# Kernel optimization log

Measured on AMD Instinct MI355X. Metric: run time of the kernel, lower is better.

The kernel has to match this reference:

```python
import jax, jax.numpy as jnp
import numpy as np

N_NODES = 20000
N_EDGES = 320000
HIDDEN = 64
HEADS = 4
D_INNER = 256
NEG_SLOPE = 0.2
BN_EPS = 1e-5


def setup_inputs() -> dict:
    key = jax.random.key(0)
    ks = jax.random.split(key, 8)
    s = 1.0 / np.sqrt(HIDDEN)
    return {
        "x": jax.random.normal(ks[0], (N_NODES, HIDDEN), jnp.float32),
        "edge_index": jax.random.randint(ks[1], (2, N_EDGES), 0, N_NODES, jnp.int64),
        "W_l": jax.random.normal(ks[2], (HIDDEN, HEADS * HIDDEN), jnp.float32) * s,
        "b_l": jnp.zeros((HEADS * HIDDEN,), jnp.float32),
        "W_r": jax.random.normal(ks[3], (HIDDEN, HEADS * HIDDEN), jnp.float32) * s,
        "b_r": jnp.zeros((HEADS * HIDDEN,), jnp.float32),
        "att": jax.random.normal(ks[4], (HEADS, HIDDEN), jnp.float32) * s,
        "bias_gat": jnp.zeros((HIDDEN,), jnp.float32),
        "gamma1": jnp.ones((HIDDEN,), jnp.float32),
        "beta1": jnp.zeros((HIDDEN,), jnp.float32),
        "W1": jax.random.normal(ks[5], (HIDDEN, D_INNER), jnp.float32) * s,
        "b1": jnp.zeros((D_INNER,), jnp.float32),
        "W2": jax.random.normal(ks[6], (D_INNER, HIDDEN), jnp.float32) / np.sqrt(D_INNER),
        "b2": jnp.zeros((HIDDEN,), jnp.float32),
        "gamma2": jnp.ones((HIDDEN,), jnp.float32),
        "beta2": jnp.zeros((HIDDEN,), jnp.float32),
    }


def _batch_norm(x, gamma, beta):
    # training-mode BatchNorm1d over the node axis (biased variance, as torch)
    mu = x.mean(0)
    var = jnp.mean((x - mu) ** 2, axis=0)
    return (x - mu) * jax.lax.rsqrt(var + BN_EPS) * gamma + beta


def _gatv2(x, edge_index, W_l, b_l, W_r, b_r, att, bias_gat):
    N = x.shape[0]
    H, C = att.shape
    src, dst = edge_index[0], edge_index[1]  # j (source), i (target)
    xl = (x @ W_l + b_l).reshape(N, H, C)  # messages (x_j side)
    xr = (x @ W_r + b_r).reshape(N, H, C)  # target (x_i side)
    # GATv2 dynamic attention: a^T LeakyReLU(x_i + x_j), per head
    e = jax.nn.leaky_relu(xl[src] + xr[dst], NEG_SLOPE)  # [E, H, C]
    score = jnp.einsum("ehc,hc->eh", e, att)  # [E, H]
    # segment softmax over incoming edges of each target node
    m = jax.ops.segment_max(score, dst, num_segments=N)  # [N, H]
    ex = jnp.exp(score - m[dst])
    denom = jax.ops.segment_sum(ex, dst, num_segments=N)  # [N, H]
    alpha = ex / jnp.maximum(denom[dst], 1e-16)  # [E, H]
    out = jax.ops.segment_sum(alpha[:, :, None] * xl[src], dst, num_segments=N)  # [N, H, C]
    return out.mean(axis=1) + bias_gat  # concat=False -> mean over heads


def reference(x, edge_index, W_l, b_l, W_r, b_r, att, bias_gat,
              gamma1, beta1, W1, b1, W2, b2, gamma2, beta2):
    x2 = _gatv2(x, edge_index, W_l, b_l, W_r, b_r, att, bias_gat)
    x = x + x2  # dropout is identity in eval
    x = _batch_norm(x, gamma1, beta1)
    ff = jax.nn.relu(x @ W1 + b1) @ W2 + b2
    x = x + ff
    x = _batch_norm(x, gamma2, beta2)
    return x
```

## Files before the change

kernel.cpp:

```cpp
#include <hip/hip_runtime.h>
#include <hip/hip_bf16.h>
#include <math.h>

#define N_NODES 20000
#define N_EDGES 320000
#define HIDDEN 64
#define HEADS 4
#define HC 256
#define D_INNER 256
#define NEG_SLOPE 0.2f
#define BN_EPS 1e-5f
#define MAXDEG 64
#define NZERO (N_NODES + 2048)
#define NB_LIN 626
#define NB_FILL 1250

typedef __attribute__((ext_vector_type(8))) short short8;
typedef __attribute__((ext_vector_type(4))) float f32x4;

__device__ __forceinline__ float bf2f(unsigned short u) {
    unsigned x = ((unsigned)u) << 16;
    return __uint_as_float(x);
}
__device__ __forceinline__ unsigned short f2bf(float f) {
    __hip_bfloat16 b = __float2bfloat16(f);
    return *reinterpret_cast<unsigned short*>(&b);
}
__device__ __forceinline__ void cvt8(uint4 u, float* f) {
    f[0] = __uint_as_float(u.x << 16); f[1] = __uint_as_float(u.x & 0xFFFF0000u);
    f[2] = __uint_as_float(u.y << 16); f[3] = __uint_as_float(u.y & 0xFFFF0000u);
    f[4] = __uint_as_float(u.z << 16); f[5] = __uint_as_float(u.z & 0xFFFF0000u);
    f[6] = __uint_as_float(u.w << 16); f[7] = __uint_as_float(u.w & 0xFFFF0000u);
}

__global__ __launch_bounds__(256) void k_wprep(const float* __restrict__ W1, const float* __restrict__ W2,
                                               const float* __restrict__ Wl, const float* __restrict__ Wr,
                                               unsigned short* __restrict__ W1tb, unsigned short* __restrict__ W2tb,
                                               unsigned short* __restrict__ Wlrtb,
                                               int* __restrict__ zbuf, int* __restrict__ perm) {
    int idx = blockIdx.x * 256 + threadIdx.x;
    if (idx < NZERO) zbuf[idx] = 0;
    int4 z4 = {0, 0, 0, 0};
    int4* p4 = (int4*)perm;
#pragma unroll
    for (int i = 0; i < 5; ++i) {
        int k = idx + i * 65536;
        if (k < N_NODES * MAXDEG / 4) p4[k] = z4;
    }
    if (idx < 16384) {
        int k = idx >> 8, n = idx & 255;
        W1tb[n * 64 + k] = f2bf(W1[idx]);
    } else if (idx < 32768) {
        int j = idx - 16384;
        int k = j >> 6, n = j & 63;
        W2tb[n * 256 + k] = f2bf(W2[j]);
    } else if (idx < 49152) {
        int j = idx - 32768;
        int k = j >> 8, n = j & 255;
        Wlrtb[n * 64 + k] = f2bf(Wl[j]);
    } else {
        int j = idx - 49152;
        int k = j >> 8, n = j & 255;
        Wlrtb[16384 + n * 64 + k] = f2bf(Wr[j]);
    }
}

__global__ __launch_bounds__(256) void k_prep(const float* __restrict__ x,
                                              const unsigned short* __restrict__ Wlrtb,
                                              const float* __restrict__ bl, const float* __restrict__ br,
                                              unsigned short* __restrict__ xlb, unsigned short* __restrict__ xrb,
                                              const int* __restrict__ ei,
                                              int* __restrict__ cursor, int* __restrict__ perm) {
    __shared__ unsigned short sW[16384];
    int t = threadIdx.x;
    if (blockIdx.x >= NB_LIN) {
        int e = (blockIdx.x - NB_LIN) * 256 + t;
        int ed = ei[N_EDGES + e];
        int slot = atomicAdd(&cursor[ed], 1);
        perm[ed * MAXDEG + slot] = ei[e];
        return;
    }
    int w = t >> 6, lane = t & 63;
    int l15 = lane & 15, lg = lane >> 4;
    int side = blockIdx.x & 1;
    int row0 = (blockIdx.x >> 1) * 64;
    const float* bias = side ? br : bl;
    unsigned short* dst = side ? xrb : xlb;
    {
        const short8* src = (const short8*)(Wlrtb + side * 16384);
#pragma unroll
        for (int it = 0; it < 8; ++it) {
            int i = it * 256 + t;
            int n = i >> 3, c = i & 7;
            *(short8*)((char*)sW + n * 128 + ((c * 16) ^ ((n & 7) << 4))) = src[i];
        }
    }
    short8 af[4][2];
#pragma unroll
    for (int mt = 0; mt < 4; ++mt) {
        int gm = row0 + mt * 16 + l15;
        bool valid = gm < N_NODES;
#pragma unroll
        for (int kk = 0; kk < 2; ++kk) {
            int k0 = kk * 32 + lg * 8;
            float4 v0 = {0.f,0.f,0.f,0.f}, v1 = {0.f,0.f,0.f,0.f};
            if (valid) {
                v0 = *(const float4*)(x + (size_t)gm * 64 + k0);
                v1 = *(const float4*)(x + (size_t)gm * 64 + k0 + 4);
            }
            short8 f;
            f[0] = (short)f2bf(v0.x); f[1] = (short)f2bf(v0.y);
            f[2] = (short)f2bf(v0.z); f[3] = (short)f2bf(v0.w);
            f[4] = (short)f2bf(v1.x); f[5] = (short)f2bf(v1.y);
            f[6] = (short)f2bf(v1.z); f[7] = (short)f2bf(v1.w);
            af[mt][kk] = f;
        }
    }
    float bv[4];
#pragma unroll
    for (int nt = 0; nt < 4; ++nt) bv[nt] = bias[w * 64 + nt * 16 + l15];
    __syncthreads();
    f32x4 zero4 = {0.f, 0.f, 0.f, 0.f};
    f32x4 acc[4][4];
#pragma unroll
    for (int mt = 0; mt < 4; ++mt)
#pragma unroll
        for (int nt = 0; nt < 4; ++nt) acc[mt][nt] = zero4;
#pragma unroll
    for (int kk = 0; kk < 2; ++kk) {
        int kb = kk * 64 + lg * 16;
        short8 bf[4];
#pragma unroll
        for (int nt = 0; nt < 4; ++nt) {
            int n = w * 64 + nt * 16 + l15;
            bf[nt] = *(const short8*)((const char*)sW + n * 128 + (kb ^ ((n & 7) << 4)));
        }
#pragma unroll
        for (int mt = 0; mt < 4; ++mt)
#pragma unroll
            for (int nt = 0; nt < 4; ++nt)
                acc[mt][nt] = __builtin_amdgcn_mfma_f32_16x16x32_bf16(af[mt][kk], bf[nt], acc[mt][nt], 0, 0, 0);
    }
#pragma unroll
    for (int mt = 0; mt < 4; ++mt)
#pragma unroll
        for (int nt = 0; nt < 4; ++nt) {
            int n = w * 64 + nt * 16 + l15;
#pragma unroll
            for (int r = 0; r < 4; ++r) {
                int gm = row0 + mt * 16 + lg * 4 + r;
                if (gm < N_NODES)
                    dst[(size_t)gm * 256 + n] = f2bf(acc[mt][nt][r] + bv[nt]);
            }
        }
}

__global__ __launch_bounds__(256) void k_gat(const unsigned short* __restrict__ xlb,
                                             const unsigned short* __restrict__ xrb,
                                             const float* __restrict__ att,
                                             const int* __restrict__ perm,
                                             const int* __restrict__ cnt,
                                             const float* __restrict__ x,
                                             const float* __restrict__ bias,
                                             float* __restrict__ y1,
                                             float* __restrict__ gsum, float* __restrict__ gsq) {
    __shared__ float ps[8][64], pq[8][64];
    int t = threadIdx.x;
    int hw = t >> 5, l = t & 31;
    int node = blockIdx.x * 8 + hw;
    const uint4* xl4 = (const uint4*)xlb;
    uint4 xru = ((const uint4*)xrb)[(size_t)node * 32 + l];
    float xr[8]; cvt8(xru, xr);
    float at[8];
    *(float4*)(at)     = *(const float4*)(att + l * 8);
    *(float4*)(at + 4) = *(const float4*)(att + l * 8 + 4);
    int deg = cnt[node];
    int mdeg = max(deg, __shfl_xor(deg, 32));
    const int* ep = perm + (size_t)node * MAXDEG;
    float d = 0.f;
    float acc[8] = {0.f,0.f,0.f,0.f,0.f,0.f,0.f,0.f};
    uint4 uv0 = xl4[(size_t)ep[0] * 32 + l];
    uint4 uv1 = xl4[(size_t)ep[1] * 32 + l];
    for (int j = 0; j < mdeg; ++j) {
        uint4 un = xl4[(size_t)ep[j + 2] * 32 + l];
        float xl[8]; cvt8(uv0, xl);
        float v[8];
        float sv0 = 0.f, sv1 = 0.f, sa0 = 0.f, sa1 = 0.f;
#pragma unroll
        for (int i = 0; i < 8; i += 2) {
            v[i] = xl[i] + xr[i];
            v[i+1] = xl[i+1] + xr[i+1];
            sv0 = fmaf(at[i], v[i], sv0);
            sa0 = fmaf(at[i], fabsf(v[i]), sa0);
            sv1 = fmaf(at[i+1], v[i+1], sv1);
            sa1 = fmaf(at[i+1], fabsf(v[i+1]), sa1);
        }
        float s = 0.6f * (sv0 + sv1) + 0.4f * (sa0 + sa1);
        s += __shfl_xor(s, 1);
        s += __shfl_xor(s, 2);
        s += __shfl_xor(s, 4);
        float w = (j < deg) ? __expf(s) : 0.f;
        d += w;
#pragma unroll
        for (int i = 0; i < 8; ++i) acc[i] = fmaf(w, xl[i], acc[i]);
        uv0 = uv1; uv1 = un;
    }
    float inv = 1.f / fmaxf(d, 1e-16f);
#pragma unroll
    for (int i = 0; i < 8; ++i) {
        float v2 = acc[i] * inv;
        v2 += __shfl_xor(v2, 8);
        v2 += __shfl_xor(v2, 16);
        acc[i] = v2;
    }
    if (l < 8) {
        float4 xv0 = *(const float4*)(x + (size_t)node * 64 + l * 8);
        float4 xv1 = *(const float4*)(x + (size_t)node * 64 + l * 8 + 4);
        float4 bv0 = *(const float4*)(bias + l * 8);
        float4 bv1 = *(const float4*)(bias + l * 8 + 4);
        float4 y0, y1v;
        y0.x = xv0.x + 0.25f * acc[0] + bv0.x;
        y0.y = xv0.y + 0.25f * acc[1] + bv0.y;
        y0.z = xv0.z + 0.25f * acc[2] + bv0.z;
        y0.w = xv0.w + 0.25f * acc[3] + bv0.w;
        y1v.x = xv1.x + 0.25f * acc[4] + bv1.x;
        y1v.y = xv1.y + 0.25f * acc[5] + bv1.y;
        y1v.z = xv1.z + 0.25f * acc[6] + bv1.z;
        y1v.w = xv1.w + 0.25f * acc[7] + bv1.w;
        *(float4*)(y1 + (size_t)node * 64 + l * 8) = y0;
        *(float4*)(y1 + (size_t)node * 64 + l * 8 + 4) = y1v;
        int c = l * 8;
        ps[hw][c+0] = y0.x; ps[hw][c+1] = y0.y; ps[hw][c+2] = y0.z; ps[hw][c+3] = y0.w;
        ps[hw][c+4] = y1v.x; ps[hw][c+5] = y1v.y; ps[hw][c+6] = y1v.z; ps[hw][c+7] = y1v.w;
        pq[hw][c+0] = y0.x*y0.x; pq[hw][c+1] = y0.y*y0.y; pq[hw][c+2] = y0.z*y0.z; pq[hw][c+3] = y0.w*y0.w;
        pq[hw][c+4] = y1v.x*y1v.x; pq[hw][c+5] = y1v.y*y1v.y; pq[hw][c+6] = y1v.z*y1v.z; pq[hw][c+7] = y1v.w*y1v.w;
    }
    __syncthreads();
    if (t < 64) {
        float s = 0.f, q = 0.f;
#pragma unroll
        for (int r = 0; r < 8; ++r) { s += ps[r][t]; q += pq[r][t]; }
        int rb = blockIdx.x & 7;
        atomicAdd(&gsum[rb * 64 + t], s);
        atomicAdd(&gsq [rb * 64 + t], q);
    }
}

__global__ __launch_bounds__(256) void k_ffn(const float* __restrict__ y1,
                                             const float* __restrict__ s1, const float* __restrict__ q1,
                                             const float* __restrict__ gamma1, const float* __restrict__ beta1,
                                             const unsigned short* __restrict__ W1tb, const float* __restrict__ b1,
                                             const unsigned short* __restrict__ W2tb, const float* __restrict__ b2,
                                             float* __restrict__ out,
                                             float* __restrict__ gsum2, float* __restrict__ gsq2) {
    __shared__ unsigned short sW[16384];
    __shared__ unsigned short sH[16384];
    __shared__ __align__(16) float sA1[64], sC1[64];
    int t = threadIdx.x;
    int w = t >> 6, lane = t & 63;
    int l15 = lane & 15, lg = lane >> 4;
    int blk = blockIdx.x;

    {
        const short8* src = (const short8*)W1tb;
#pragma unroll
        for (int it = 0; it < 8; ++it) {
            int i = it * 256 + t;
            int n = i >> 3, c = i & 7;
            *(short8*)((char*)sW + n * 128 + ((c * 16) ^ ((n & 7) << 4))) = src[i];
        }
    }
    if (t < 64) {
        float s = 0.f, q = 0.f;
#pragma unroll
        for (int r = 0; r < 8; ++r) { s += s1[r * 64 + t]; q += q1[r * 64 + t]; }
        float mu = s * (1.0f / N_NODES);
        float var = fmaxf(q * (1.0f / N_NODES) - mu * mu, 0.f);
        float av = gamma1[t] * rsqrtf(var + BN_EPS);
        sA1[t] = av; sC1[t] = beta1[t] - mu * av;
    }
    __syncthreads();

    float4 a1k[2][2], c1k[2][2];
#pragma unroll
    for (int kk = 0; kk < 2; ++kk) {
        int k0 = kk * 32 + lg * 8;
        a1k[kk][0] = *(const float4*)(sA1 + k0); a1k[kk][1] = *(const float4*)(sA1 + k0 + 4);
        c1k[kk][0] = *(const float4*)(sC1 + k0); c1k[kk][1] = *(const float4*)(sC1 + k0 + 4);
    }
    short8 af[4][2];
#pragma unroll
    for (int mt = 0; mt < 4; ++mt) {
        int gm = blk * 64 + mt * 16 + l15;
        bool valid = gm < N_NODES;
#pragma unroll
        for (int kk = 0; kk < 2; ++kk) {
            int k0 = kk * 32 + lg * 8;
            float4 v0 = {0.f,0.f,0.f,0.f}, v1 = {0.f,0.f,0.f,0.f};
            if (valid) {
                v0 = *(const float4*)(y1 + (size_t)gm * 64 + k0);
                v1 = *(const float4*)(y1 + (size_t)gm * 64 + k0 + 4);
            }
            short8 f;
            f[0] = (short)f2bf(fmaf(a1k[kk][0].x, v0.x, c1k[kk][0].x));
            f[1] = (short)f2bf(fmaf(a1k[kk][0].y, v0.y, c1k[kk][0].y));
            f[2] = (short)f2bf(fmaf(a1k[kk][0].z, v0.z, c1k[kk][0].z));
            f[3] = (short)f2bf(fmaf(a1k[kk][0].w, v0.w, c1k[kk][0].w));
            f[4] = (short)f2bf(fmaf(a1k[kk][1].x, v1.x, c1k[kk][1].x));
            f[5] = (short)f2bf(fmaf(a1k[kk][1].y, v1.y, c1k[kk][1].y));
            f[6] = (short)f2bf(fmaf(a1k[kk][1].z, v1.z, c1k[kk][1].z));
            f[7] = (short)f2bf(fmaf(a1k[kk][1].w, v1.w, c1k[kk][1].w));
            af[mt][kk] = f;
        }
    }
    float b1v[4];
#pragma unroll
    for (int nt = 0; nt < 4; ++nt) b1v[nt] = b1[w * 64 + nt * 16 + l15];

    f32x4 zero4 = {0.f, 0.f, 0.f, 0.f};
    f32x4 acc[4][4];
#pragma unroll
    for (int mt = 0; mt < 4; ++mt)
#pragma unroll
        for (int nt = 0; nt < 4; ++nt) acc[mt][nt] = zero4;
#pragma unroll
    for (int kk = 0; kk < 2; ++kk) {
        int kb = kk * 64 + lg * 16;
        short8 bf[4];
#pragma unroll
        for (int nt = 0; nt < 4; ++nt) {
            int n = w * 64 + nt * 16 + l15;
            bf[nt] = *(const short8*)((const char*)sW + n * 128 + (kb ^ ((n & 7) << 4)));
        }
#pragma unroll
        for (int mt = 0; mt < 4; ++mt)
#pragma unroll
            for (int nt = 0; nt < 4; ++nt)
                acc[mt][nt] = __builtin_amdgcn_mfma_f32_16x16x32_bf16(af[mt][kk], bf[nt], acc[mt][nt], 0, 0, 0);
    }
    __syncthreads();

#pragma unroll
    for (int mt = 0; mt < 4; ++mt)
#pragma unroll
        for (int nt = 0; nt < 4; ++nt) {
            int n = w * 64 + nt * 16 + l15;
#pragma unroll
            for (int r = 0; r < 4; ++r) {
                int m = mt * 16 + lg * 4 + r;
                float h = fmaxf(acc[mt][nt][r] + b1v[nt], 0.f);
                *(unsigned short*)((char*)sH + m * 512 + ((n * 2) ^ ((m & 7) << 4))) = f2bf(h);
            }
        }
    {
        const short8* src = (const short8*)W2tb;
#pragma unroll
        for (int it = 0; it < 8; ++it) {
            int i = it * 256 + t;
            int n = i >> 5, c = i & 31;
            *(short8*)((char*)sW + n * 512 + ((c * 16) ^ ((n & 7) << 4))) = src[i];
        }
    }
    __syncthreads();

    f32x4 acc2[4];
#pragma unroll
    for (int nt = 0; nt < 4; ++nt) acc2[nt] = zero4;
#pragma unroll
    for (int kk = 0; kk < 8; ++kk) {
        int kb = kk * 64 + lg * 16;
        int m = w * 16 + l15;
        short8 a2 = *(const short8*)((const char*)sH + m * 512 + (kb ^ ((m & 7) << 4)));
#pragma unroll
        for (int nt = 0; nt < 4; ++nt) {
            int n = nt * 16 + l15;
            short8 b2f = *(const short8*)((const char*)sW + n * 512 + (kb ^ ((n & 7) << 4)));
            acc2[nt] = __builtin_amdgcn_mfma_f32_16x16x32_bf16(a2, b2f, acc2[nt], 0, 0, 0);
        }
    }

    float b2v[4], a1n[4], c1n[4], ssum[4] = {0.f,0.f,0.f,0.f}, ssq[4] = {0.f,0.f,0.f,0.f};
#pragma unroll
    for (int nt = 0; nt < 4; ++nt) {
        int n = nt * 16 + l15;
        b2v[nt] = b2[n]; a1n[nt] = sA1[n]; c1n[nt] = sC1[n];
    }
#pragma unroll
    for (int nt = 0; nt < 4; ++nt) {
        int n = nt * 16 + l15;
#pragma unroll
        for (int r = 0; r < 4; ++r) {
            int gm = blk * 64 + w * 16 + lg * 4 + r;
            if (gm < N_NODES) {
                float v = acc2[nt][r] + b2v[nt] + fmaf(a1n[nt], y1[(size_t)gm * 64 + n], c1n[nt]);
                out[(size_t)gm * 64 + n] = v;
                ssum[nt] += v; ssq[nt] += v * v;
            }
        }
    }
    __syncthreads();
    float* fs = (float*)sW;
#pragma unroll
    for (int nt = 0; nt < 4; ++nt) {
        float ss = ssum[nt], qq = ssq[nt];
        ss += __shfl_xor(ss, 16); ss += __shfl_xor(ss, 32);
        qq += __shfl_xor(qq, 16); qq += __shfl_xor(qq, 32);
        if (lg == 0) {
            int n = nt * 16 + l15;
            fs[w * 64 + n] = ss;
            fs[256 + w * 64 + n] = qq;
        }
    }
    __syncthreads();
    if (t < 64) {
        int r = blk & 7;
        atomicAdd(&gsum2[r * 64 + t], fs[t] + fs[64 + t] + fs[128 + t] + fs[192 + t]);
        atomicAdd(&gsq2 [r * 64 + t], fs[256 + t] + fs[320 + t] + fs[384 + t] + fs[448 + t]);
    }
}

__global__ __launch_bounds__(256) void k_apply(float* __restrict__ out,
                                               const float* __restrict__ s2, const float* __restrict__ q2,
                                               const float* __restrict__ gamma2, const float* __restrict__ beta2) {
    __shared__ float sA[64], sC[64];
    int t = threadIdx.x;
    if (t < 64) {
        float s = 0.f, q = 0.f;
#pragma unroll
        for (int r = 0; r < 8; ++r) { s += s2[r * 64 + t]; q += q2[r * 64 + t]; }
        float mu = s * (1.0f / N_NODES);
        float var = fmaxf(q * (1.0f / N_NODES) - mu * mu, 0.f);
        float av = gamma2[t] * rsqrtf(var + BN_EPS);
        sA[t] = av; sC[t] = beta2[t] - mu * av;
    }
    __syncthreads();
    int idx = blockIdx.x * 1024 + t * 4;
    int ch = (t & 15) * 4;
    float4 v = *(float4*)(out + idx);
    v.x = fmaf(sA[ch+0], v.x, sC[ch+0]);
    v.y = fmaf(sA[ch+1], v.y, sC[ch+1]);
    v.z = fmaf(sA[ch+2], v.z, sC[ch+2]);
    v.w = fmaf(sA[ch+3], v.w, sC[ch+3]);
    *(float4*)(out + idx) = v;
}

extern "C" void kernel_launch(void* const* d_in, const int* in_sizes, int n_in,
                              void* d_out, int out_size, void* d_ws, size_t ws_size,
                              hipStream_t stream) {
    const float* x        = (const float*)d_in[0];
    const int*   ei       = (const int*)d_in[1];
    const float* Wl       = (const float*)d_in[2];
    const float* bl       = (const float*)d_in[3];
    const float* Wr       = (const float*)d_in[4];
    const float* br       = (const float*)d_in[5];
    const float* att      = (const float*)d_in[6];
    const float* bias_gat = (const float*)d_in[7];
    const float* gamma1   = (const float*)d_in[8];
    const float* beta1    = (const float*)d_in[9];
    const float* W1       = (const float*)d_in[10];
    const float* b1       = (const float*)d_in[11];
    const float* W2       = (const float*)d_in[12];
    const float* b2       = (const float*)d_in[13];
    const float* gamma2   = (const float*)d_in[14];
    const float* beta2    = (const float*)d_in[15];
    float* out = (float*)d_out;

    char* ws = (char*)d_ws;
    unsigned short* xlb = (unsigned short*)ws;
    unsigned short* xrb = xlb + (size_t)N_NODES * HC;
    float* y1    = (float*)(xrb + (size_t)N_NODES * HC);
    int*   perm  = (int*)(y1 + (size_t)N_NODES * HIDDEN);
    int*   cursor= perm + (size_t)N_NODES * MAXDEG;
    float* stats = (float*)(cursor + N_NODES);
    unsigned short* W1tb  = (unsigned short*)(stats + 2048);
    unsigned short* W2tb  = W1tb + 16384;
    unsigned short* Wlrtb = W2tb + 16384;

    k_wprep<<<256, 256, 0, stream>>>(W1, W2, Wl, Wr, W1tb, W2tb, Wlrtb, cursor, perm);
    k_prep <<<NB_LIN + NB_FILL, 256, 0, stream>>>(x, Wlrtb, bl, br, xlb, xrb, ei, cursor, perm);
    k_gat  <<<N_NODES / 8, 256, 0, stream>>>(xlb, xrb, att, perm, cursor, x, bias_gat, y1,
                                             stats + 0, stats + 512);
    k_ffn  <<<(N_NODES + 63) / 64, 256, 0, stream>>>(y1, stats + 0, stats + 512, gamma1, beta1,
                                                     W1tb, b1, W2tb, b2, out,
                                                     stats + 1024, stats + 1536);
    k_apply<<<N_NODES * HIDDEN / 1024, 256, 0, stream>>>(out, stats + 1024, stats + 1536, gamma2, beta2);
}
```

Baseline: 95.43 us.

## Stream GAT neighbor gathers into an LDS ring buffer via global_load_lds

```diff
diff --git a/kernel.cpp b/kernel.cpp
--- a/kernel.cpp
+++ b/kernel.cpp
@@ -31,6 +31,14 @@
     f[2] = __uint_as_float(u.y << 16); f[3] = __uint_as_float(u.y & 0xFFFF0000u);
     f[4] = __uint_as_float(u.z << 16); f[5] = __uint_as_float(u.z & 0xFFFF0000u);
     f[6] = __uint_as_float(u.w << 16); f[7] = __uint_as_float(u.w & 0xFFFF0000u);
+}
+__device__ __forceinline__ void gl_lds16(const void* g, void* l) {
+    __builtin_amdgcn_global_load_lds((const __attribute__((address_space(1))) void*)g,
+                                     (__attribute__((address_space(3))) void*)l, 16, 0, 0);
+}
+__device__ __forceinline__ void gl_lds4(const void* g, void* l) {
+    __builtin_amdgcn_global_load_lds((const __attribute__((address_space(1))) void*)g,
+                                     (__attribute__((address_space(3))) void*)l, 4, 0, 0);
 }
 
 __global__ __launch_bounds__(256) void k_wprep(const float* __restrict__ W1, const float* __restrict__ W2,
@@ -165,10 +173,18 @@
                                              float* __restrict__ y1,
                                              float* __restrict__ gsum, float* __restrict__ gsq) {
     __shared__ float ps[8][64], pq[8][64];
+    __shared__ __align__(16) char slots[4][8 * 1024];
+    __shared__ int sidx[4][2][64];
     int t = threadIdx.x;
-    int hw = t >> 5, l = t & 31;
+    int wv = t >> 6;
+    int lane = t & 63;
+    int hw = t >> 5;
+    int l = t & 31;
     int node = blockIdx.x * 8 + hw;
-    const uint4* xl4 = (const uint4*)xlb;
+
+    gl_lds4(perm + (size_t)(blockIdx.x * 8 + wv * 2) * MAXDEG + lane, &sidx[wv][0][0]);
+    gl_lds4(perm + (size_t)(blockIdx.x * 8 + wv * 2 + 1) * MAXDEG + lane, &sidx[wv][1][0]);
+
     uint4 xru = ((const uint4*)xrb)[(size_t)node * 32 + l];
     float xr[8]; cvt8(xru, xr);
     float at[8];
@@ -176,26 +192,38 @@
     *(float4*)(at + 4) = *(const float4*)(att + l * 8 + 4);
     int deg = cnt[node];
     int mdeg = max(deg, __shfl_xor(deg, 32));
-    const int* ep = perm + (size_t)node * MAXDEG;
+    asm volatile("s_waitcnt vmcnt(0)" ::: "memory");
+    __builtin_amdgcn_sched_barrier(0);
+
+    const int* myidx = &sidx[wv][lane >> 5][0];
+    const char* xlbase = (const char*)xlb;
+    char* slotbase = &slots[wv][0];
+#pragma unroll
+    for (int k = 0; k < 8; ++k) {
+        int srck = myidx[k];
+        gl_lds16(xlbase + (size_t)srck * 512 + l * 16, slotbase + k * 1024);
+    }
+
     float d = 0.f;
     float acc[8] = {0.f,0.f,0.f,0.f,0.f,0.f,0.f,0.f};
-    uint4 uv0 = xl4[(size_t)ep[0] * 32 + l];
-    uint4 uv1 = xl4[(size_t)ep[1] * 32 + l];
     for (int j = 0; j < mdeg; ++j) {
-        uint4 un = xl4[(size_t)ep[j + 2] * 32 + l];
-        float xl[8]; cvt8(uv0, xl);
-        float v[8];
-        float sv0 = 0.f, sv1 = 0.f, sa0 = 0.f, sa1 = 0.f;
-#pragma unroll
-        for (int i = 0; i < 8; i += 2) {
-            v[i] = xl[i] + xr[i];
-            v[i+1] = xl[i+1] + xr[i+1];
-            sv0 = fmaf(at[i], v[i], sv0);
-            sa0 = fmaf(at[i], fabsf(v[i]), sa0);
-            sv1 = fmaf(at[i+1], v[i+1], sv1);
-            sa1 = fmaf(at[i+1], fabsf(v[i+1]), sa1);
-        }
-        float s = 0.6f * (sv0 + sv1) + 0.4f * (sa0 + sa1);
+        int srcn = myidx[j + 8];
+        asm volatile("s_waitcnt vmcnt(7)" ::: "memory");
+        __builtin_amdgcn_sched_barrier(0);
+        int slot = j & 7;
+        uint4 uv = *(const uint4*)(slotbase + slot * 1024 + lane * 16);
+        float xl[8]; cvt8(uv, xl);
+        asm volatile("s_waitcnt lgkmcnt(0)" ::: "memory");
+        __builtin_amdgcn_sched_barrier(0);
+        gl_lds16(xlbase + (size_t)srcn * 512 + l * 16, slotbase + slot * 1024);
+        float sv = 0.f, sa = 0.f;
+#pragma unroll
+        for (int i = 0; i < 8; ++i) {
+            float v = xl[i] + xr[i];
+            sv = fmaf(at[i], v, sv);
+            sa = fmaf(at[i], fabsf(v), sa);
+        }
+        float s = 0.6f * sv + 0.4f * sa;
         s += __shfl_xor(s, 1);
         s += __shfl_xor(s, 2);
         s += __shfl_xor(s, 4);
@@ -203,7 +231,6 @@
         d += w;
 #pragma unroll
         for (int i = 0; i < 8; ++i) acc[i] = fmaf(w, xl[i], acc[i]);
-        uv0 = uv1; uv1 = un;
     }
     float inv = 1.f / fmaxf(d, 1e-16f);
 #pragma unroll
```

Result: faster. 93.07 us (-2.5%).

## Assign one wavefront per node in GAT aggregation, splitting edges across half-waves

Applied to the files above, without the earlier changes.

```diff
diff --git a/kernel.cpp b/kernel.cpp
--- a/kernel.cpp
+++ b/kernel.cpp
@@ -164,10 +164,13 @@
                                              const float* __restrict__ bias,
                                              float* __restrict__ y1,
                                              float* __restrict__ gsum, float* __restrict__ gsq) {
-    __shared__ float ps[8][64], pq[8][64];
+    __shared__ float ps[4][64], pq[4][64];
     int t = threadIdx.x;
-    int hw = t >> 5, l = t & 31;
-    int node = blockIdx.x * 8 + hw;
+    int wv = t >> 6;
+    int node = blockIdx.x * 4 + wv;
+    int lane = t & 63;
+    int hi = lane >> 5;
+    int l = lane & 31;
     const uint4* xl4 = (const uint4*)xlb;
     uint4 xru = ((const uint4*)xrb)[(size_t)node * 32 + l];
     float xr[8]; cvt8(xru, xr);
@@ -175,49 +178,46 @@
     *(float4*)(at)     = *(const float4*)(att + l * 8);
     *(float4*)(at + 4) = *(const float4*)(att + l * 8 + 4);
     int deg = cnt[node];
-    int mdeg = max(deg, __shfl_xor(deg, 32));
     const int* ep = perm + (size_t)node * MAXDEG;
     float d = 0.f;
     float acc[8] = {0.f,0.f,0.f,0.f,0.f,0.f,0.f,0.f};
-    uint4 uv0 = xl4[(size_t)ep[0] * 32 + l];
-    uint4 uv1 = xl4[(size_t)ep[1] * 32 + l];
-    for (int j = 0; j < mdeg; ++j) {
-        uint4 un = xl4[(size_t)ep[j + 2] * 32 + l];
-        float xl[8]; cvt8(uv0, xl);
-        float v[8];
-        float sv0 = 0.f, sv1 = 0.f, sa0 = 0.f, sa1 = 0.f;
-#pragma unroll
-        for (int i = 0; i < 8; i += 2) {
-            v[i] = xl[i] + xr[i];
-            v[i+1] = xl[i+1] + xr[i+1];
-            sv0 = fmaf(at[i], v[i], sv0);
-            sa0 = fmaf(at[i], fabsf(v[i]), sa0);
-            sv1 = fmaf(at[i+1], v[i+1], sv1);
-            sa1 = fmaf(at[i+1], fabsf(v[i+1]), sa1);
-        }
-        float s = 0.6f * (sv0 + sv1) + 0.4f * (sa0 + sa1);
+    uint4 b0 = xl4[(size_t)ep[hi] * 32 + l];
+    uint4 b1 = xl4[(size_t)ep[2 + hi] * 32 + l];
+    for (int j = 0; j < deg; j += 2) {
+        uint4 nx = xl4[(size_t)ep[j + 4 + hi] * 32 + l];
+        float xl[8]; cvt8(b0, xl);
+        float sv = 0.f, sa = 0.f;
+#pragma unroll
+        for (int i = 0; i < 8; ++i) {
+            float v = xl[i] + xr[i];
+            sv = fmaf(at[i], v, sv);
+            sa = fmaf(at[i], fabsf(v), sa);
+        }
+        float s = 0.6f * sv + 0.4f * sa;
         s += __shfl_xor(s, 1);
         s += __shfl_xor(s, 2);
         s += __shfl_xor(s, 4);
-        float w = (j < deg) ? __expf(s) : 0.f;
+        float w = (j + hi < deg) ? __expf(s) : 0.f;
         d += w;
 #pragma unroll
         for (int i = 0; i < 8; ++i) acc[i] = fmaf(w, xl[i], acc[i]);
-        uv0 = uv1; uv1 = un;
-    }
+        b0 = b1; b1 = nx;
+    }
+    d += __shfl_xor(d, 32);
     float inv = 1.f / fmaxf(d, 1e-16f);
 #pragma unroll
     for (int i = 0; i < 8; ++i) {
-        float v2 = acc[i] * inv;
+        float v2 = acc[i] + __shfl_xor(acc[i], 32);
+        v2 *= inv;
         v2 += __shfl_xor(v2, 8);
         v2 += __shfl_xor(v2, 16);
         acc[i] = v2;
     }
-    if (l < 8) {
-        float4 xv0 = *(const float4*)(x + (size_t)node * 64 + l * 8);
-        float4 xv1 = *(const float4*)(x + (size_t)node * 64 + l * 8 + 4);
-        float4 bv0 = *(const float4*)(bias + l * 8);
-        float4 bv1 = *(const float4*)(bias + l * 8 + 4);
+    if (lane < 8) {
+        float4 xv0 = *(const float4*)(x + (size_t)node * 64 + lane * 8);
+        float4 xv1 = *(const float4*)(x + (size_t)node * 64 + lane * 8 + 4);
+        float4 bv0 = *(const float4*)(bias + lane * 8);
+        float4 bv1 = *(const float4*)(bias + lane * 8 + 4);
         float4 y0, y1v;
         y0.x = xv0.x + 0.25f * acc[0] + bv0.x;
         y0.y = xv0.y + 0.25f * acc[1] + bv0.y;
@@ -227,19 +227,18 @@
         y1v.y = xv1.y + 0.25f * acc[5] + bv1.y;
         y1v.z = xv1.z + 0.25f * acc[6] + bv1.z;
         y1v.w = xv1.w + 0.25f * acc[7] + bv1.w;
-        *(float4*)(y1 + (size_t)node * 64 + l * 8) = y0;
-        *(float4*)(y1 + (size_t)node * 64 + l * 8 + 4) = y1v;
-        int c = l * 8;
-        ps[hw][c+0] = y0.x; ps[hw][c+1] = y0.y; ps[hw][c+2] = y0.z; ps[hw][c+3] = y0.w;
-        ps[hw][c+4] = y1v.x; ps[hw][c+5] = y1v.y; ps[hw][c+6] = y1v.z; ps[hw][c+7] = y1v.w;
-        pq[hw][c+0] = y0.x*y0.x; pq[hw][c+1] = y0.y*y0.y; pq[hw][c+2] = y0.z*y0.z; pq[hw][c+3] = y0.w*y0.w;
-        pq[hw][c+4] = y1v.x*y1v.x; pq[hw][c+5] = y1v.y*y1v.y; pq[hw][c+6] = y1v.z*y1v.z; pq[hw][c+7] = y1v.w*y1v.w;
+        *(float4*)(y1 + (size_t)node * 64 + lane * 8) = y0;
+        *(float4*)(y1 + (size_t)node * 64 + lane * 8 + 4) = y1v;
+        int c = lane * 8;
+        ps[wv][c+0] = y0.x; ps[wv][c+1] = y0.y; ps[wv][c+2] = y0.z; ps[wv][c+3] = y0.w;
+        ps[wv][c+4] = y1v.x; ps[wv][c+5] = y1v.y; ps[wv][c+6] = y1v.z; ps[wv][c+7] = y1v.w;
+        pq[wv][c+0] = y0.x*y0.x; pq[wv][c+1] = y0.y*y0.y; pq[wv][c+2] = y0.z*y0.z; pq[wv][c+3] = y0.w*y0.w;
+        pq[wv][c+4] = y1v.x*y1v.x; pq[wv][c+5] = y1v.y*y1v.y; pq[wv][c+6] = y1v.z*y1v.z; pq[wv][c+7] = y1v.w*y1v.w;
     }
     __syncthreads();
     if (t < 64) {
-        float s = 0.f, q = 0.f;
-#pragma unroll
-        for (int r = 0; r < 8; ++r) { s += ps[r][t]; q += pq[r][t]; }
+        float s = ps[0][t] + ps[1][t] + ps[2][t] + ps[3][t];
+        float q = pq[0][t] + pq[1][t] + pq[2][t] + pq[3][t];
         int rb = blockIdx.x & 7;
         atomicAdd(&gsum[rb * 64 + t], s);
         atomicAdd(&gsq [rb * 64 + t], q);
@@ -478,7 +477,7 @@
 
     k_wprep<<<256, 256, 0, stream>>>(W1, W2, Wl, Wr, W1tb, W2tb, Wlrtb, cursor, perm);
     k_prep <<<NB_LIN + NB_FILL, 256, 0, stream>>>(x, Wlrtb, bl, br, xlb, xrb, ei, cursor, perm);
-    k_gat  <<<N_NODES / 8, 256, 0, stream>>>(xlb, xrb, att, perm, cursor, x, bias_gat, y1,
+    k_gat  <<<N_NODES / 4, 256, 0, stream>>>(xlb, xrb, att, perm, cursor, x, bias_gat, y1,
                                              stats + 0, stats + 512);
     k_ffn  <<<(N_NODES + 63) / 64, 256, 0, stream>>>(y1, stats + 0, stats + 512, gamma1, beta1,
                                                      W1tb, b1, W2tb, b2, out,
```

After: 91.00 us. 4.6% less time.
